# Kernel optimization log

Measured on AMD Instinct MI355X. Metric: run time of the kernel, lower is better.

Reference implementation:

```python
import jax, jax.numpy as jnp
import numpy as np

D_MODEL = 1024
N_HEADS = 16
HEAD_DIM = D_MODEL // N_HEADS


def setup_inputs() -> dict:
    key = jax.random.key(0)
    ks = jax.random.split(key, 5)
    B, T = 4, 2048
    x = jax.random.normal(ks[0], (B, T, D_MODEL), dtype=jnp.float32)
    s = 0.02
    W_qkv = jax.random.normal(ks[1], (D_MODEL, 3 * D_MODEL), dtype=jnp.float32) * s
    b_qkv = jnp.zeros((3 * D_MODEL,), dtype=jnp.float32)
    W_out = jax.random.normal(ks[2], (D_MODEL, D_MODEL), dtype=jnp.float32) * s
    b_out = jnp.zeros((D_MODEL,), dtype=jnp.float32)
    return {"x": x, "W_qkv": W_qkv, "b_qkv": b_qkv, "W_out": W_out, "b_out": b_out}


def reference(x, W_qkv, b_qkv, W_out, b_out):
    B, T, C = x.shape
    H, Dh = N_HEADS, HEAD_DIM
    qkv = x @ W_qkv + b_qkv                      # [B,T,3C]
    q, k, v = jnp.split(qkv, 3, axis=-1)
    q = q.reshape(B, T, H, Dh).transpose(0, 2, 1, 3)  # [B,H,T,Dh]
    k = k.reshape(B, T, H, Dh).transpose(0, 2, 1, 3)
    v = v.reshape(B, T, H, Dh).transpose(0, 2, 1, 3)
    scale = 1.0 / jnp.sqrt(jnp.float32(Dh))
    scores = jnp.einsum('bhqd,bhkd->bhqk', q, k) * scale  # [B,H,T,T]
    causal = jnp.tril(jnp.ones((T, T), dtype=bool))
    scores = jnp.where(causal[None, None], scores, jnp.float32(-jnp.inf))
    w = jax.nn.softmax(scores, axis=-1)
    y = jnp.einsum('bhqk,bhkd->bhqd', w, v)      # [B,H,T,Dh]
    y = y.transpose(0, 2, 1, 3).reshape(B, T, C)
    return y @ W_out + b_out
```

## Files before the change

kernel.cpp:

```cpp
#include <hip/hip_runtime.h>
#include <cstdint>
#include <math.h>

#define TT 2048
#define CC 1024
#define HH 16
#define DH 64
#define BB 4
#define MM 8192

typedef unsigned short u16;
typedef __bf16 bf16_t;
typedef bf16_t bf16x8 __attribute__((ext_vector_type(8)));
typedef float f32x4 __attribute__((ext_vector_type(4)));

static __device__ inline u16 f2bf(float f) {
    unsigned int u = __builtin_bit_cast(unsigned int, f);
    unsigned int lsb = (u >> 16) & 1u;
    u += 0x7fffu + lsb;
    return (u16)(u >> 16);
}

static __device__ inline unsigned int cvt_pk_bf16(float a, float b) {
    unsigned int r;
    asm volatile("v_cvt_pk_bf16_f32 %0, %1, %2" : "=v"(r) : "v"(a), "v"(b));
    return r;
}

#define GLL16(gptr, lptr)                                                            \
    __builtin_amdgcn_global_load_lds(                                                \
        (__attribute__((address_space(1))) void*)(gptr),                             \
        (__attribute__((address_space(3))) void*)(lptr), 16, 0, 0)


__global__ void cast_x_kernel(const float* __restrict__ x, u16* __restrict__ xb, int n4) {
    int i = blockIdx.x * blockDim.x + threadIdx.x;
    if (i >= n4) return;
    float4 v = ((const float4*)x)[i];
    uint2 o;
    o.x = cvt_pk_bf16(v.x, v.y);
    o.y = cvt_pk_bf16(v.z, v.w);
    ((uint2*)xb)[i] = o;
}

__global__ void __launch_bounds__(256)
transpose_cast_kernel(const float* __restrict__ W, u16* __restrict__ Wt, int K, int N) {
    __shared__ u16 tile[32 * 34];
    const int tx = threadIdx.x & 31;
    const int ty = threadIdx.x >> 5;
    const int n0 = blockIdx.x * 32;
    const int k0 = blockIdx.y * 32;
#pragma unroll
    for (int i = 0; i < 4; ++i) {
        int k = ty + i * 8;
        tile[tx * 34 + k] = f2bf(W[(size_t)(k0 + k) * N + n0 + tx]);
    }
    __syncthreads();
    const int tx2 = threadIdx.x & 15;
    const int ty2 = threadIdx.x >> 4;
#pragma unroll
    for (int i = 0; i < 2; ++i) {
        int r = ty2 + i * 16;
        *(unsigned int*)&Wt[(size_t)(n0 + r) * K + k0 + 2 * tx2] =
            *(unsigned int*)&tile[r * 34 + 2 * tx2];
    }
}

template <int MODE>
__global__ void __launch_bounds__(256)
gemm_bt_kernel(const u16* __restrict__ A, const u16* __restrict__ Bt,
               const float* __restrict__ bias, float* __restrict__ Cout,
               u16* __restrict__ qws, u16* __restrict__ kws, u16* __restrict__ vtws,
               int Mdim, int Ndim, int Kdim) {
    __shared__ u16 As[2][128 * 32];
    __shared__ u16 Bs[2][128 * 32];

    const int tid  = threadIdx.x;
    const int w    = tid >> 6;
    const int lane = tid & 63;
    const int l15  = lane & 15;
    const int quad = lane >> 4;
    const int wm   = (w & 1) * 64;
    const int wn   = (w >> 1) * 64;
    const int m0   = blockIdx.y * 128;
    const int n0   = blockIdx.x * 128;

    const int row0  = tid >> 2;
    const int row1  = row0 + 64;
    const int col8  = (tid & 3) << 3;

    f32x4 acc[4][4];
#pragma unroll
    for (int i = 0; i < 4; ++i)
#pragma unroll
        for (int j = 0; j < 4; ++j) acc[i][j] = (f32x4){0.f, 0.f, 0.f, 0.f};

    auto stageA = [&](int buf, int kc) {
        if (MODE == 0) {
            int kcc = kc + col8, h = kcc >> 6, d = kcc & 63;
            int m = m0 + row0, b = m >> 11, t = m & 2047;
            GLL16(&A[(((size_t)(b * HH + h) * TT + t) * DH) + d], &As[buf][tid * 8]);
            m = m0 + row1; b = m >> 11; t = m & 2047;
            GLL16(&A[(((size_t)(b * HH + h) * TT + t) * DH) + d], &As[buf][(tid + 256) * 8]);
        } else {
            GLL16(&A[(size_t)(m0 + row0) * Kdim + kc + col8], &As[buf][tid * 8]);
            GLL16(&A[(size_t)(m0 + row1) * Kdim + kc + col8], &As[buf][(tid + 256) * 8]);
        }
    };

    stageA(0, 0);
    GLL16(&Bt[(size_t)(n0 + row0) * Kdim + col8], &Bs[0][tid * 8]);
    GLL16(&Bt[(size_t)(n0 + row1) * Kdim + col8], &Bs[0][(tid + 256) * 8]);

    const int nsteps = Kdim >> 5;
    for (int it = 0; it < nsteps; ++it) {
        const int buf = it & 1;
        __syncthreads();

        if (it + 1 < nsteps) {
            const int nbuf = buf ^ 1;
            const int kc = (it + 1) << 5;
            stageA(nbuf, kc);
            GLL16(&Bt[(size_t)(n0 + row0) * Kdim + kc + col8], &Bs[nbuf][tid * 8]);
            GLL16(&Bt[(size_t)(n0 + row1) * Kdim + kc + col8], &Bs[nbuf][(tid + 256) * 8]);
        }

        bf16x8 af[4], bfm[4];
#pragma unroll
        for (int mt = 0; mt < 4; ++mt)
            af[mt] = *(const bf16x8*)&As[buf][(wm + mt * 16 + l15) * 32 + quad * 8];
#pragma unroll
        for (int nt = 0; nt < 4; ++nt)
            bfm[nt] = *(const bf16x8*)&Bs[buf][(wn + nt * 16 + l15) * 32 + quad * 8];
#pragma unroll
        for (int mt = 0; mt < 4; ++mt)
#pragma unroll
            for (int nt = 0; nt < 4; ++nt)
                acc[mt][nt] = __builtin_amdgcn_mfma_f32_16x16x32_bf16(
                    af[mt], bfm[nt], acc[mt][nt], 0, 0, 0);
    }

#pragma unroll
    for (int mt = 0; mt < 4; ++mt) {
        int mrow_base = m0 + wm + mt * 16 + quad * 4;
#pragma unroll
        for (int nt = 0; nt < 4; ++nt) {
            int ncol = n0 + wn + nt * 16 + l15;
            float bv = bias[ncol];
            if (MODE == 0) {
#pragma unroll
                for (int r = 0; r < 4; ++r)
                    Cout[(size_t)(mrow_base + r) * Ndim + ncol] = acc[mt][nt][r] + bv;
            } else {
                int which = ncol >> 10, c = ncol & 1023;
                int h = c >> 6, d = c & 63;
                if (which == 2) {
                    int b = mrow_base >> 11, t = mrow_base & 2047;
                    int bh = b * HH + h;
                    uint2 pv;
                    pv.x = cvt_pk_bf16(acc[mt][nt][0] + bv, acc[mt][nt][1] + bv);
                    pv.y = cvt_pk_bf16(acc[mt][nt][2] + bv, acc[mt][nt][3] + bv);
                    *(uint2*)&vtws[((size_t)bh * DH + d) * TT + t] = pv;
                } else {
#pragma unroll
                    for (int r = 0; r < 4; ++r) {
                        int mrow = mrow_base + r;
                        int b = mrow >> 11, t = mrow & 2047;
                        int bh = b * HH + h;
                        float val = acc[mt][nt][r] + bv;
                        if (which == 0) {
                            qws[((size_t)bh * TT + t) * DH + d] = f2bf(val * 0.18033688f);
                        } else {
                            kws[((size_t)bh * TT + t) * DH + d] = f2bf(val);
                        }
                    }
                }
            }
        }
    }
}

__global__ void __launch_bounds__(256, 3)
attn_kernel(const u16* __restrict__ qws, const u16* __restrict__ kws,
            const u16* __restrict__ vtws, u16* __restrict__ yws) {
    __shared__ u16 Ks[2][64 * 68];
    __shared__ u16 Vs[2][64 * 68];
    __shared__ u16 Ps[4][32 * 68];

    const int tid  = threadIdx.x;
    const int w    = tid >> 6;
    const int lane = tid & 63;
    const int l15  = lane & 15;
    const int quad = lane >> 4;
    const int bh   = blockIdx.x;
    const int qt   = 15 - blockIdx.y;

    const u16* Kbase = kws + (size_t)bh * TT * DH;
    const u16* Vbase = vtws + (size_t)bh * DH * TT;
    u16* Pw = &Ps[w][0];

    const int srow  = tid >> 2;
    const int sc16  = (tid & 3) << 4;

    bf16x8 aones;
#pragma unroll
    for (int i = 0; i < 8; ++i) aones[i] = __builtin_bit_cast(bf16_t, (u16)0x3F80);

    const int q0     = qt * 128;
    const int qr0    = q0 + w * 32;
    const int ntiles = (q0 + 128) >> 6;

    const u16* Qp = qws + ((size_t)bh * TT + qr0) * DH;
    bf16x8 bqa[2], bqb[2];
#pragma unroll
    for (int kk = 0; kk < 2; ++kk) {
        bqa[kk] = *(const bf16x8*)&Qp[l15 * DH + kk * 32 + quad * 8];
        bqb[kk] = *(const bf16x8*)&Qp[(16 + l15) * DH + kk * 32 + quad * 8];
    }

    f32x4 o[2][4], ol[2];
#pragma unroll
    for (int qg = 0; qg < 2; ++qg) {
#pragma unroll
        for (int dt = 0; dt < 4; ++dt) o[qg][dt] = (f32x4){0.f, 0.f, 0.f, 0.f};
        ol[qg] = (f32x4){0.f, 0.f, 0.f, 0.f};
    }

    uint4 pk0 = *(const uint4*)&Kbase[(size_t)srow * DH + sc16];
    uint4 pk1 = *(const uint4*)&Kbase[(size_t)srow * DH + sc16 + 8];
    uint4 pv0 = *(const uint4*)&Vbase[(size_t)srow * TT + sc16];
    uint4 pv1 = *(const uint4*)&Vbase[(size_t)srow * TT + sc16 + 8];
    *(uint4*)&Ks[0][srow * 68 + sc16]     = pk0;
    *(uint4*)&Ks[0][srow * 68 + sc16 + 8] = pk1;
    *(uint4*)&Vs[0][srow * 68 + sc16]     = pv0;
    *(uint4*)&Vs[0][srow * 68 + sc16 + 8] = pv1;
    if (ntiles > 1) {
        pk0 = *(const uint4*)&Kbase[(size_t)(64 + srow) * DH + sc16];
        pk1 = *(const uint4*)&Kbase[(size_t)(64 + srow) * DH + sc16 + 8];
        pv0 = *(const uint4*)&Vbase[(size_t)srow * TT + 64 + sc16];
        pv1 = *(const uint4*)&Vbase[(size_t)srow * TT + 64 + sc16 + 8];
    }

    for (int it = 0; it < ntiles; ++it) {
        const int buf = it & 1;
        __syncthreads();

        if (it + 1 < ntiles) {
            *(uint4*)&Ks[buf ^ 1][srow * 68 + sc16]     = pk0;
            *(uint4*)&Ks[buf ^ 1][srow * 68 + sc16 + 8] = pk1;
            *(uint4*)&Vs[buf ^ 1][srow * 68 + sc16]     = pv0;
            *(uint4*)&Vs[buf ^ 1][srow * 68 + sc16 + 8] = pv1;
            if (it + 2 < ntiles) {
                int jn = (it + 2) << 6;
                pk0 = *(const uint4*)&Kbase[(size_t)(jn + srow) * DH + sc16];
                pk1 = *(const uint4*)&Kbase[(size_t)(jn + srow) * DH + sc16 + 8];
                pv0 = *(const uint4*)&Vbase[(size_t)srow * TT + jn + sc16];
                pv1 = *(const uint4*)&Vbase[(size_t)srow * TT + jn + sc16 + 8];
            }
        }

        const int j0 = it << 6;
        if (j0 > qr0 + 31) continue;

        bf16x8 ak[8];
#pragma unroll
        for (int kk = 0; kk < 2; ++kk)
#pragma unroll
            for (int kt = 0; kt < 4; ++kt)
                ak[kk * 4 + kt] =
                    *(const bf16x8*)&Ks[buf][(kt * 16 + l15) * 68 + kk * 32 + quad * 8];

        f32x4 sa[4], sb[4];
#pragma unroll
        for (int kt = 0; kt < 4; ++kt) {
            sa[kt] = (f32x4){0.f, 0.f, 0.f, 0.f};
            sb[kt] = (f32x4){0.f, 0.f, 0.f, 0.f};
        }
#pragma unroll
        for (int kk = 0; kk < 2; ++kk)
#pragma unroll
            for (int kt = 0; kt < 4; ++kt)
                sa[kt] = __builtin_amdgcn_mfma_f32_16x16x32_bf16(ak[kk * 4 + kt], bqa[kk], sa[kt], 0, 0, 0);
#pragma unroll
        for (int kk = 0; kk < 2; ++kk)
#pragma unroll
            for (int kt = 0; kt < 4; ++kt)
                sb[kt] = __builtin_amdgcn_mfma_f32_16x16x32_bf16(ak[kk * 4 + kt], bqb[kk], sb[kt], 0, 0, 0);

        if (j0 + 63 > qr0) {
            int qy0 = qr0 + l15;
            int qy1 = qr0 + 16 + l15;
#pragma unroll
            for (int kt = 0; kt < 4; ++kt)
#pragma unroll
                for (int r = 0; r < 4; ++r) {
                    int key = j0 + kt * 16 + quad * 4 + r;
                    if (key > qy0) sa[kt][r] = -INFINITY;
                    if (key > qy1) sb[kt][r] = -INFINITY;
                }
        }

#pragma unroll
        for (int kt = 0; kt < 4; ++kt)
#pragma unroll
            for (int r = 0; r < 4; ++r) {
                sa[kt][r] = __builtin_amdgcn_exp2f(sa[kt][r]);
                sb[kt][r] = __builtin_amdgcn_exp2f(sb[kt][r]);
            }

        bf16x8 avr[8];
#pragma unroll
        for (int kk = 0; kk < 2; ++kk)
#pragma unroll
            for (int dt = 0; dt < 4; ++dt)
                avr[kk * 4 + dt] =
                    *(const bf16x8*)&Vs[buf][(dt * 16 + l15) * 68 + kk * 32 + quad * 8];

#pragma unroll
        for (int kt = 0; kt < 4; ++kt) {
            uint2 pda, pdb;
            pda.x = cvt_pk_bf16(sa[kt][0], sa[kt][1]);
            pda.y = cvt_pk_bf16(sa[kt][2], sa[kt][3]);
            pdb.x = cvt_pk_bf16(sb[kt][0], sb[kt][1]);
            pdb.y = cvt_pk_bf16(sb[kt][2], sb[kt][3]);
            *(uint2*)&Pw[l15 * 68 + kt * 16 + quad * 4]        = pda;
            *(uint2*)&Pw[(16 + l15) * 68 + kt * 16 + quad * 4] = pdb;
        }
        asm volatile("s_waitcnt lgkmcnt(0)" ::: "memory");

#pragma unroll
        for (int qg = 0; qg < 2; ++qg) {
            bf16x8 bp0 = *(const bf16x8*)&Pw[(qg * 16 + l15) * 68 + quad * 8];
            bf16x8 bp1 = *(const bf16x8*)&Pw[(qg * 16 + l15) * 68 + 32 + quad * 8];
#pragma unroll
            for (int dt = 0; dt < 4; ++dt)
                o[qg][dt] = __builtin_amdgcn_mfma_f32_16x16x32_bf16(avr[dt], bp0, o[qg][dt], 0, 0, 0);
            ol[qg] = __builtin_amdgcn_mfma_f32_16x16x32_bf16(aones, bp0, ol[qg], 0, 0, 0);
#pragma unroll
            for (int dt = 0; dt < 4; ++dt)
                o[qg][dt] = __builtin_amdgcn_mfma_f32_16x16x32_bf16(avr[4 + dt], bp1, o[qg][dt], 0, 0, 0);
            ol[qg] = __builtin_amdgcn_mfma_f32_16x16x32_bf16(aones, bp1, ol[qg], 0, 0, 0);
        }
    }

#pragma unroll
    for (int qg = 0; qg < 2; ++qg) {
        float rinv = __builtin_amdgcn_rcpf(ol[qg][0]);
        int t = qr0 + qg * 16 + l15;
#pragma unroll
        for (int dt = 0; dt < 4; ++dt) {
            uint2 yv;
            yv.x = cvt_pk_bf16(o[qg][dt][0] * rinv, o[qg][dt][1] * rinv);
            yv.y = cvt_pk_bf16(o[qg][dt][2] * rinv, o[qg][dt][3] * rinv);
            *(uint2*)&yws[((size_t)bh * TT + t) * DH + dt * 16 + quad * 4] = yv;
        }
    }
}


extern "C" void kernel_launch(void* const* d_in, const int* in_sizes, int n_in,
                              void* d_out, int out_size, void* d_ws, size_t ws_size,
                              hipStream_t stream) {
    const float* x     = (const float*)d_in[0];
    const float* W_qkv = (const float*)d_in[1];
    const float* b_qkv = (const float*)d_in[2];
    const float* W_out = (const float*)d_in[3];
    const float* b_out = (const float*)d_in[4];
    float* out = (float*)d_out;

    char* ws = (char*)d_ws;
    u16* xb   = (u16*)ws; ws += (size_t)MM * CC * 2;
    u16* wqt  = (u16*)ws; ws += (size_t)3 * CC * CC * 2;
    u16* wot  = (u16*)ws; ws += (size_t)CC * CC * 2;
    u16* qws  = (u16*)ws; ws += (size_t)MM * CC * 2;
    u16* kws  = (u16*)ws; ws += (size_t)MM * CC * 2;
    u16* vtws = (u16*)ws; ws += (size_t)MM * CC * 2;
    u16* yws  = (u16*)ws; ws += (size_t)MM * CC * 2;

    cast_x_kernel<<<(MM * CC / 4) / 256, 256, 0, stream>>>(x, xb, MM * CC / 4);
    transpose_cast_kernel<<<dim3(3 * CC / 32, CC / 32), 256, 0, stream>>>(W_qkv, wqt, CC, 3 * CC);
    transpose_cast_kernel<<<dim3(CC / 32, CC / 32), 256, 0, stream>>>(W_out, wot, CC, CC);

    gemm_bt_kernel<1><<<dim3(24, 64), 256, 0, stream>>>(
        xb, wqt, b_qkv, nullptr, qws, kws, vtws, MM, 3 * CC, CC);

    attn_kernel<<<dim3(BB * HH, 16), 256, 0, stream>>>(qws, kws, vtws, yws);

    gemm_bt_kernel<0><<<dim3(8, 64), 256, 0, stream>>>(
        yws, wot, b_out, out, nullptr, nullptr, nullptr, MM, CC, CC);
}
```

Measured before the change: 272.5 us.

## Keep softmax probabilities in registers by permuting V layout, drop P LDS staging

The V-transpose store in the QKV GEMM epilogue now permutes time indices within each 64-block, so the MFMA output layout of the score tile lines up directly with the B-operand layout for the PV MFMA. The probabilities are packed to bf16 in registers and fed straight into the PV MFMAs, which removes the per-wave shared-memory P buffer, its write/read round trip and the lgkmcnt wait. With less LDS in use, the launch bound is raised to 4 blocks per CU and the V fragment loads are moved earlier to overlap with the QK MFMAs. The permutation has to match the MFMA lane mapping exactly or results will be wrong, and the higher occupancy target may force register spilling.

```diff
diff --git a/kernel.cpp b/kernel.cpp
--- a/kernel.cpp
+++ b/kernel.cpp
@@ -157,10 +157,13 @@
                 if (which == 2) {
                     int b = mrow_base >> 11, t = mrow_base & 2047;
                     int bh = b * HH + h;
+                    int ch = (t >> 2) & 15;
+                    int chp = (ch & 8) | (((ch >> 1) & 1) << 2) | ((ch & 1) << 1) | ((ch >> 2) & 1);
+                    int tp = (t & ~63) | (chp << 2);
                     uint2 pv;
                     pv.x = cvt_pk_bf16(acc[mt][nt][0] + bv, acc[mt][nt][1] + bv);
                     pv.y = cvt_pk_bf16(acc[mt][nt][2] + bv, acc[mt][nt][3] + bv);
-                    *(uint2*)&vtws[((size_t)bh * DH + d) * TT + t] = pv;
+                    *(uint2*)&vtws[((size_t)bh * DH + d) * TT + tp] = pv;
                 } else {
 #pragma unroll
                     for (int r = 0; r < 4; ++r) {
@@ -180,12 +183,11 @@
     }
 }
 
-__global__ void __launch_bounds__(256, 3)
+__global__ void __launch_bounds__(256, 4)
 attn_kernel(const u16* __restrict__ qws, const u16* __restrict__ kws,
             const u16* __restrict__ vtws, u16* __restrict__ yws) {
     __shared__ u16 Ks[2][64 * 68];
     __shared__ u16 Vs[2][64 * 68];
-    __shared__ u16 Ps[4][32 * 68];
 
     const int tid  = threadIdx.x;
     const int w    = tid >> 6;
@@ -197,7 +199,6 @@
 
     const u16* Kbase = kws + (size_t)bh * TT * DH;
     const u16* Vbase = vtws + (size_t)bh * DH * TT;
-    u16* Pw = &Ps[w][0];
 
     const int srow  = tid >> 2;
     const int sc16  = (tid & 3) << 4;
@@ -270,6 +271,14 @@
                 ak[kk * 4 + kt] =
                     *(const bf16x8*)&Ks[buf][(kt * 16 + l15) * 68 + kk * 32 + quad * 8];
 
+        bf16x8 avr[8];
+#pragma unroll
+        for (int kk = 0; kk < 2; ++kk)
+#pragma unroll
+            for (int dt = 0; dt < 4; ++dt)
+                avr[kk * 4 + dt] =
+                    *(const bf16x8*)&Vs[buf][(dt * 16 + l15) * 68 + kk * 32 + quad * 8];
+
         f32x4 sa[4], sb[4];
 #pragma unroll
         for (int kt = 0; kt < 4; ++kt) {
@@ -308,39 +317,44 @@
                 sb[kt][r] = __builtin_amdgcn_exp2f(sb[kt][r]);
             }
 
-        bf16x8 avr[8];
-#pragma unroll
-        for (int kk = 0; kk < 2; ++kk)
-#pragma unroll
-            for (int dt = 0; dt < 4; ++dt)
-                avr[kk * 4 + dt] =
-                    *(const bf16x8*)&Vs[buf][(dt * 16 + l15) * 68 + kk * 32 + quad * 8];
-
-#pragma unroll
-        for (int kt = 0; kt < 4; ++kt) {
-            uint2 pda, pdb;
-            pda.x = cvt_pk_bf16(sa[kt][0], sa[kt][1]);
-            pda.y = cvt_pk_bf16(sa[kt][2], sa[kt][3]);
-            pdb.x = cvt_pk_bf16(sb[kt][0], sb[kt][1]);
-            pdb.y = cvt_pk_bf16(sb[kt][2], sb[kt][3]);
-            *(uint2*)&Pw[l15 * 68 + kt * 16 + quad * 4]        = pda;
-            *(uint2*)&Pw[(16 + l15) * 68 + kt * 16 + quad * 4] = pdb;
-        }
-        asm volatile("s_waitcnt lgkmcnt(0)" ::: "memory");
-
-#pragma unroll
-        for (int qg = 0; qg < 2; ++qg) {
-            bf16x8 bp0 = *(const bf16x8*)&Pw[(qg * 16 + l15) * 68 + quad * 8];
-            bf16x8 bp1 = *(const bf16x8*)&Pw[(qg * 16 + l15) * 68 + 32 + quad * 8];
-#pragma unroll
-            for (int dt = 0; dt < 4; ++dt)
-                o[qg][dt] = __builtin_amdgcn_mfma_f32_16x16x32_bf16(avr[dt], bp0, o[qg][dt], 0, 0, 0);
-            ol[qg] = __builtin_amdgcn_mfma_f32_16x16x32_bf16(aones, bp0, ol[qg], 0, 0, 0);
-#pragma unroll
-            for (int dt = 0; dt < 4; ++dt)
-                o[qg][dt] = __builtin_amdgcn_mfma_f32_16x16x32_bf16(avr[4 + dt], bp1, o[qg][dt], 0, 0, 0);
-            ol[qg] = __builtin_amdgcn_mfma_f32_16x16x32_bf16(aones, bp1, ol[qg], 0, 0, 0);
-        }
+        uint4 ua0, ua1, ub0, ub1;
+        ua0.x = cvt_pk_bf16(sa[0][0], sa[0][1]);
+        ua0.y = cvt_pk_bf16(sa[0][2], sa[0][3]);
+        ua0.z = cvt_pk_bf16(sa[1][0], sa[1][1]);
+        ua0.w = cvt_pk_bf16(sa[1][2], sa[1][3]);
+        ua1.x = cvt_pk_bf16(sa[2][0], sa[2][1]);
+        ua1.y = cvt_pk_bf16(sa[2][2], sa[2][3]);
+        ua1.z = cvt_pk_bf16(sa[3][0], sa[3][1]);
+        ua1.w = cvt_pk_bf16(sa[3][2], sa[3][3]);
+        ub0.x = cvt_pk_bf16(sb[0][0], sb[0][1]);
+        ub0.y = cvt_pk_bf16(sb[0][2], sb[0][3]);
+        ub0.z = cvt_pk_bf16(sb[1][0], sb[1][1]);
+        ub0.w = cvt_pk_bf16(sb[1][2], sb[1][3]);
+        ub1.x = cvt_pk_bf16(sb[2][0], sb[2][1]);
+        ub1.y = cvt_pk_bf16(sb[2][2], sb[2][3]);
+        ub1.z = cvt_pk_bf16(sb[3][0], sb[3][1]);
+        ub1.w = cvt_pk_bf16(sb[3][2], sb[3][3]);
+        bf16x8 bpa0 = __builtin_bit_cast(bf16x8, ua0);
+        bf16x8 bpa1 = __builtin_bit_cast(bf16x8, ua1);
+        bf16x8 bpb0 = __builtin_bit_cast(bf16x8, ub0);
+        bf16x8 bpb1 = __builtin_bit_cast(bf16x8, ub1);
+
+#pragma unroll
+        for (int dt = 0; dt < 4; ++dt)
+            o[0][dt] = __builtin_amdgcn_mfma_f32_16x16x32_bf16(avr[dt], bpa0, o[0][dt], 0, 0, 0);
+        ol[0] = __builtin_amdgcn_mfma_f32_16x16x32_bf16(aones, bpa0, ol[0], 0, 0, 0);
+#pragma unroll
+        for (int dt = 0; dt < 4; ++dt)
+            o[0][dt] = __builtin_amdgcn_mfma_f32_16x16x32_bf16(avr[4 + dt], bpa1, o[0][dt], 0, 0, 0);
+        ol[0] = __builtin_amdgcn_mfma_f32_16x16x32_bf16(aones, bpa1, ol[0], 0, 0, 0);
+#pragma unroll
+        for (int dt = 0; dt < 4; ++dt)
+            o[1][dt] = __builtin_amdgcn_mfma_f32_16x16x32_bf16(avr[dt], bpb0, o[1][dt], 0, 0, 0);
+        ol[1] = __builtin_amdgcn_mfma_f32_16x16x32_bf16(aones, bpb0, ol[1], 0, 0, 0);
+#pragma unroll
+        for (int dt = 0; dt < 4; ++dt)
+            o[1][dt] = __builtin_amdgcn_mfma_f32_16x16x32_bf16(avr[4 + dt], bpb1, o[1][dt], 0, 0, 0);
+        ol[1] = __builtin_amdgcn_mfma_f32_16x16x32_bf16(aones, bpb1, ol[1], 0, 0, 0);
     }
 
 #pragma unroll
```

New measurement: 375.9 us. 37.9% more time.
